# Optimization experiments

Measured on AMD Instinct MI355X. Metric: run time of the kernel, lower is better.

The kernel has to match this reference:

```python
import jax, jax.numpy as jnp
import numpy as np

B, N, DIM = 2, 16384, 512
H, D = 8, 64          # heads, dim_head
M = 64                # n_global_queries
SC, DC = 64, 64       # context slices, context_dim


def _linear(x, W, b):
    return x @ W.T + b


def setup_inputs() -> dict:
    key = jax.random.key(0)
    ks = jax.random.split(key, 12)
    def w(k, shape, fan_in):
        return jax.random.normal(k, shape, jnp.float32) / np.sqrt(fan_in)
    return {
        "x": jax.random.normal(ks[0], (B, N, DIM), jnp.float32),
        "context": jax.random.normal(ks[1], (B, H, SC, DC), jnp.float32),
        "q_global": jax.random.normal(ks[2], (1, H, M, D), jnp.float32),
        "Wx": w(ks[3], (H * D, DIM), DIM), "bx": jnp.zeros((H * D,), jnp.float32),
        "Wk": w(ks[4], (D, D), D), "bk": jnp.zeros((D,), jnp.float32),
        "Wv": w(ks[5], (D, D), D), "bv": jnp.zeros((D,), jnp.float32),
        "Wcq": w(ks[6], (D, D), D), "bcq": jnp.zeros((D,), jnp.float32),
        "Wck": w(ks[7], (D, DC), DC), "bck": jnp.zeros((D,), jnp.float32),
        "Wcv": w(ks[8], (D, DC), DC), "bcv": jnp.zeros((D,), jnp.float32),
        "state_mixing": jnp.zeros((), jnp.float32),
        "Wo": w(ks[9], (DIM, H * D), H * D), "bo": jnp.zeros((DIM,), jnp.float32),
    }


def reference(x, context, q_global, Wx, bx, Wk, bk, Wv, bv,
              Wcq, bcq, Wck, bck, Wcv, bcv, state_mixing, Wo, bo):
    scale = 1.0  # module uses self.scale = 1.0 (no 1/sqrt(d))
    b, n, _ = x.shape
    # in-projection: (B,N,C) -> (B,H,N,D)
    x_mid = _linear(x, Wx, bx).reshape(b, n, H, D).transpose(0, 2, 1, 3)

    # ---- FLARE low-rank self-attention (routing via M global queries) ----
    k = _linear(x_mid, Wk, bk)  # (B,H,N,D)
    v = _linear(x_mid, Wv, bv)  # (B,H,N,D)
    # encode: global queries attend over N tokens -> latent (B,H,M,D)
    enc = jax.nn.softmax(jnp.einsum('ghmd,bhnd->bhmn', q_global, k) * scale, axis=-1)
    latent = jnp.einsum('bhmn,bhnd->bhmd', enc, v)
    # decode: tokens (keys as queries) attend over M latents -> (B,H,N,D)
    dec = jax.nn.softmax(jnp.einsum('bhnd,ghmd->bhnm', k, q_global) * scale, axis=-1)
    self_attn = jnp.einsum('bhnm,bhmd->bhnd', dec, latent)

    # ---- cross-attention to geometry-aware context ----
    q = _linear(x_mid, Wcq, bcq)          # (B,H,N,D)
    kc = _linear(context, Wck, bck)       # (B,H,Sc,D)
    vc = _linear(context, Wcv, bcv)       # (B,H,Sc,D)
    attn = jax.nn.softmax(jnp.einsum('bhnd,bhsd->bhns', q, kc) * scale, axis=-1)
    cross_attn = jnp.einsum('bhns,bhsd->bhnd', attn, vc)

    # ---- sigmoid-gated mixing ----
    w = jax.nn.sigmoid(state_mixing)
    out = w * self_attn + (1.0 - w) * cross_attn  # (B,H,N,D)

    out = out.transpose(0, 2, 1, 3).reshape(b, n, H * D)
    return _linear(out, Wo, bo)  # (B,N,C); dropout=0 (eval)
```

## Files before the change

### kernel.cpp

```cpp
#include <hip/hip_runtime.h>


typedef unsigned short u16;
typedef __attribute__((ext_vector_type(4))) float  f32x4;
typedef __attribute__((ext_vector_type(4))) u16    u16x4;
typedef __attribute__((ext_vector_type(8))) __bf16 bf16x8;

__device__ __forceinline__ float bf2f(u16 u) {
    return __uint_as_float(((unsigned)u) << 16);
}
__device__ __forceinline__ u16 f2bf(float f) {
    unsigned u = __float_as_uint(f);
    u += 0x7fffu + ((u >> 16) & 1u);
    return (u16)(u >> 16);
}
__device__ __forceinline__ void gload16(const void* g, void* l) {
    __builtin_amdgcn_global_load_lds(
        (const __attribute__((address_space(1))) unsigned int*)g,
        (__attribute__((address_space(3))) unsigned int*)l, 16, 0, 0);
}

#define MASK_NONE 0x7fffffffu

template<int BM, int BN, int WMW, int WNW>
__device__ __forceinline__ void gemm_core(
    const u16* __restrict__ A, int lda, unsigned amask, int koffA,
    const u16* __restrict__ Bm, int ldb, unsigned bmask, int koffB,
    int K, int trow, int tcol,
    u16* As, u16* Bs,
    f32x4 (&acc)[BM / WMW / 16][BN / WNW / 16])
{
    constexpr int FM = BM / WMW / 16;
    constexpr int FN = BN / WNW / 16;
    const int tid  = threadIdx.x;
    const int wid  = tid >> 6, lane = tid & 63;
    const int wm   = wid % WMW, wn = wid / WMW;
    const int wr   = wm * (BM / WMW), wc = wn * (BN / WNW);
    const int lrow = lane & 15, lk = (lane >> 4) * 8;

    for (int kt = 0; kt < K; kt += 32) {
        __syncthreads();
#pragma unroll
        for (int i = 0; i < BM / 64; i++) {
            int c = i * 256 + tid;
            int row = c >> 2, kg = c & 3;
            unsigned kk = ((unsigned)(koffA + kt + kg * 8)) & amask;
            gload16(A + (size_t)(trow + row) * lda + kk, As + (size_t)c * 8);
        }
#pragma unroll
        for (int i = 0; i < BN / 64; i++) {
            int c = i * 256 + tid;
            int col = c >> 2, kg = c & 3;
            unsigned kk = ((unsigned)(koffB + kt + kg * 8)) & bmask;
            gload16(Bm + (size_t)(tcol + col) * ldb + kk, Bs + (size_t)c * 8);
        }
        __syncthreads();

        bf16x8 af[FM], bfr[FN];
#pragma unroll
        for (int fm = 0; fm < FM; fm++)
            af[fm] = *(const bf16x8*)&As[(wr + fm * 16 + lrow) * 32 + lk];
#pragma unroll
        for (int fn = 0; fn < FN; fn++)
            bfr[fn] = *(const bf16x8*)&Bs[(wc + fn * 16 + lrow) * 32 + lk];
#pragma unroll
        for (int fm = 0; fm < FM; fm++)
#pragma unroll
            for (int fn = 0; fn < FN; fn++)
                acc[fm][fn] = __builtin_amdgcn_mfma_f32_16x16x32_bf16(
                    af[fm], bfr[fn], acc[fm][fn], 0, 0, 0);
    }
}


__global__ void prep_x(const float* __restrict__ x, u16* __restrict__ xs)
{
    int t = blockIdx.x * 256 + threadIdx.x;
    int n = t >> 7, e4 = (t & 127) << 2;
    f32x4 v = *(const f32x4*)(x + (size_t)n * 512 + e4);
    u16x4 hi;
#pragma unroll
    for (int j = 0; j < 4; j++) hi[j] = f2bf(v[j]);
    *(u16x4*)(xs + (size_t)n * 512 + e4) = hi;
}

__global__ void prep_w(const float* Wk, const float* Wcq, const float* Wv,
                       const float* Wx, float* CKF, float* CQF, u16* wV)
{
    int idx = blockIdx.x * 256 + threadIdx.x;
    int which = idx >> 18;
    int rem = idx & 262143;
    int c = rem >> 9, e = rem & 511;
    int h = c >> 6, d = c & 63;
    const float* W = which == 0 ? Wk : (which == 1 ? Wcq : Wv);
    float s = 0.f;
#pragma unroll 8
    for (int j = 0; j < 64; j++)
        s += W[d * 64 + j] * Wx[(h * 64 + j) * 512 + e];
    if (which == 0)      CKF[(size_t)c * 512 + e] = s;
    else if (which == 1) CQF[(size_t)c * 512 + e] = s;
    else                 wV [(size_t)c * 512 + e] = f2bf(s);
}

__global__ void prep_bias(const float* Wk, const float* Wcq, const float* Wv,
                          const float* bk, const float* bcq, const float* bv,
                          const float* bx, float* biasKQ, float* biasV)
{
    int t = blockIdx.x * 256 + threadIdx.x;
    if (t < 1024) {
        const float* W  = (t < 512) ? Wk : Wcq;
        const float* bb = (t < 512) ? bk : bcq;
        int c = t & 511; int h = c >> 6, d = c & 63;
        float s = bb[d];
        for (int j = 0; j < 64; j++) s += W[d * 64 + j] * bx[h * 64 + j];
        biasKQ[t] = s;
    } else if (t < 1536) {
        int c = t - 1024; int h = c >> 6, d = c & 63;
        float s = bv[d];
        for (int j = 0; j < 64; j++) s += Wv[d * 64 + j] * bx[h * 64 + j];
        biasV[c] = s;
    }
}

__global__ void prep_ctx(const float* ctx, const float* Wck, const float* bck,
                         const float* Wcv, const float* bcv, const float* smix,
                         float* kcf, u16* vcT)
{
    int t = blockIdx.x * 256 + threadIdx.x;
    int bh = t >> 12, r = t & 4095;
    int s_ = r >> 6, d = r & 63;
    const float* crow = ctx + ((size_t)bh * 64 + s_) * 64;
    float kc = bck[d], vc = bcv[d];
#pragma unroll 8
    for (int e = 0; e < 64; e++) {
        float ce = crow[e];
        kc += ce * Wck[d * 64 + e];
        vc += ce * Wcv[d * 64 + e];
    }
    kcf[(size_t)bh * 4096 + s_ * 64 + d] = kc;
    float w = 1.f / (1.f + __expf(-smix[0]));
    int pos = (s_ & 15) * 4 + (s_ >> 4);
    vcT[(size_t)bh * 4096 + pos * 64 + d] = f2bf((1.f - w) * vc);
}

__global__ void prep_b2(const float* CKF, const float* CQF, const float* qg,
                        const float* kcf, const float* biasKQ, u16* BigB, float* CC)
{
    int idx = blockIdx.x * 256 + threadIdx.x;
    if (idx < 262144) {
        int hm = idx >> 9, e = idx & 511;
        int h = hm >> 6;
        float s = 0.f;
#pragma unroll 8
        for (int d = 0; d < 64; d++)
            s += CKF[(size_t)(h * 64 + d) * 512 + e] * qg[(size_t)hm * 64 + d];
        u16 hi = f2bf(s), lo = f2bf(s - bf2f(hi));
#pragma unroll
        for (int b = 0; b < 2; b++) {
            size_t base = (size_t)b * 1048576 + (size_t)hm * 1024;
            BigB[base + e]       = lo;
            BigB[base + 512 + e] = hi;
        }
    } else if (idx < 786432) {
        int i2 = idx - 262144;
        int r = i2 >> 9, e = i2 & 511;
        int b = r >> 9, hs = r & 511;
        int h = hs >> 6, s_ = hs & 63;
        float s = 0.f;
#pragma unroll 8
        for (int d = 0; d < 64; d++)
            s += CQF[(size_t)(h * 64 + d) * 512 + e]
               * kcf[(size_t)(b * 8 + h) * 4096 + s_ * 64 + d];
        u16 hi = f2bf(s), lo = f2bf(s - bf2f(hi));
        size_t base = (size_t)b * 1048576 + (size_t)(512 + hs) * 1024;
        BigB[base + e]       = lo;
        BigB[base + 512 + e] = hi;
    } else if (idx < 787968) {
        int t = idx - 786432;
        if (t < 512) {
            int h = t >> 6;
            float s = 0.f;
            for (int d = 0; d < 64; d++) s += biasKQ[h * 64 + d] * qg[(size_t)t * 64 + d];
            CC[t] = s; CC[1024 + t] = s;
        } else {
            int j = t - 512;
            int b = j >> 9, hs = j & 511;
            int h = hs >> 6, s_ = hs & 63;
            float s = 0.f;
            for (int d = 0; d < 64; d++)
                s += biasKQ[512 + h * 64 + d]
                   * kcf[(size_t)(b * 8 + h) * 4096 + s_ * 64 + d];
            CC[b * 1024 + 512 + hs] = s;
        }
    }
}

__global__ __launch_bounds__(256, 2) void k_vt(const u16* wV, const u16* xs,
                                               const float* biasV, u16* vT)
{
    __shared__ u16 As[128 * 32], Bs[128 * 32];
    f32x4 acc[4][4] = {};
    int b = blockIdx.z;
    int f = blockIdx.y * gridDim.x + blockIdx.x;
    int w = (f & 7) * 64 + (f >> 3);
    int trow = (w & 3) * 128;
    int tcol = (w >> 2) * 128;
    gemm_core<128, 128, 2, 2>(wV, 512, MASK_NONE, 0,
                              xs + (size_t)b * 8388608, 512, MASK_NONE, 0,
                              512, trow, tcol, As, Bs, acc);
    int tid = threadIdx.x, wid = tid >> 6, lane = tid & 63;
    int wr = (wid & 1) * 64, wc = (wid >> 1) * 64;
    int g = lane >> 4, li = lane & 15;
#pragma unroll
    for (int fm = 0; fm < 4; fm++)
#pragma unroll
        for (int fn = 0; fn < 4; fn++) {
            int col = tcol + wc + fn * 16 + li;
#pragma unroll
            for (int j = 0; j < 4; j++) {
                int a = trow + wr + fm * 16 + g * 4 + j;
                vT[((size_t)b * 512 + a) * 16384 + col] = f2bf(acc[fm][fn][j] + biasV[a]);
            }
        }
}

__global__ void k_L(const u16* xs, const u16* BigB, const float* CC,
                    u16* P12, float* DD)
{
    __shared__ u16 As[128 * 32], BsLo[128 * 32], BsHi[128 * 32];
    f32x4 acc[4][4] = {};
    int f = blockIdx.x;
    int w = (f & 7) * 256 + (f >> 3);
    int jt = w & 7, nb = w >> 3;
    int b = nb >> 7, ntile = nb & 127;
    int trow = ntile * 128, tcol = jt * 128;
    const u16* A  = xs   + (size_t)b * 8388608;
    const u16* Bm = BigB + (size_t)b * 1048576;
    int tid = threadIdx.x, wid = tid >> 6, lane = tid & 63;
    int wm = wid & 1, wn = wid >> 1;
    int wr = wm * 64, wc = wn * 64;
    int lrow = lane & 15, lk = (lane >> 4) * 8;

    for (int kt = 0; kt < 512; kt += 32) {
        __syncthreads();
#pragma unroll
        for (int i = 0; i < 2; i++) {
            int c = i * 256 + tid;
            int row = c >> 2, kg = c & 3;
            gload16(A + (size_t)(trow + row) * 512 + kt + kg * 8, As + (size_t)c * 8);
        }
#pragma unroll
        for (int i = 0; i < 2; i++) {
            int c = i * 256 + tid;
            int col = c >> 2, kg = c & 3;
            gload16(Bm + (size_t)(tcol + col) * 1024 + kt + kg * 8,
                    BsLo + (size_t)c * 8);
            gload16(Bm + (size_t)(tcol + col) * 1024 + 512 + kt + kg * 8,
                    BsHi + (size_t)c * 8);
        }
        __syncthreads();

        bf16x8 af[4], bfr[4];
#pragma unroll
        for (int fm = 0; fm < 4; fm++)
            af[fm] = *(const bf16x8*)&As[(wr + fm * 16 + lrow) * 32 + lk];
#pragma unroll
        for (int fn = 0; fn < 4; fn++)
            bfr[fn] = *(const bf16x8*)&BsLo[(wc + fn * 16 + lrow) * 32 + lk];
#pragma unroll
        for (int fm = 0; fm < 4; fm++)
#pragma unroll
            for (int fn = 0; fn < 4; fn++)
                acc[fm][fn] = __builtin_amdgcn_mfma_f32_16x16x32_bf16(
                    af[fm], bfr[fn], acc[fm][fn], 0, 0, 0);
#pragma unroll
        for (int fn = 0; fn < 4; fn++)
            bfr[fn] = *(const bf16x8*)&BsHi[(wc + fn * 16 + lrow) * 32 + lk];
#pragma unroll
        for (int fm = 0; fm < 4; fm++)
#pragma unroll
            for (int fn = 0; fn < 4; fn++)
                acc[fm][fn] = __builtin_amdgcn_mfma_f32_16x16x32_bf16(
                    af[fm], bfr[fn], acc[fm][fn], 0, 0, 0);
    }

    int g = lane >> 4, li = lane & 15;
    float cj[4];
#pragma unroll
    for (int fn = 0; fn < 4; fn++) cj[fn] = CC[b * 1024 + tcol + wc + fn * 16 + li];

    int h = jt * 2 + wn;
#pragma unroll
    for (int fm = 0; fm < 4; fm++)
#pragma unroll
        for (int j = 0; j < 4; j++) {
            float ev[4]; float dsum = 0.f;
#pragma unroll
            for (int fn = 0; fn < 4; fn++) {
                ev[fn] = __expf(acc[fm][fn][j] + cj[fn]);
                dsum += ev[fn];
            }
            dsum += __shfl_xor(dsum, 1); dsum += __shfl_xor(dsum, 2);
            dsum += __shfl_xor(dsum, 4); dsum += __shfl_xor(dsum, 8);
            float inv = 1.f / dsum;
            int row = trow + wr + fm * 16 + g * 4 + j;
            size_t pb = ((size_t)b * 16384 + row) * 1024 + tcol + wc;
            u16x4 pk;
#pragma unroll
            for (int fn = 0; fn < 4; fn++) pk[fn] = f2bf(ev[fn] * inv);
            *(u16x4*)(P12 + pb + li * 4) = pk;
            if (jt < 4 && li == 0)
                DD[(size_t)(b * 8 + h) * 16384 + row] = dsum;
        }
}

__global__ void k_dene(const u16* P12, const float* DD, float* denp)
{
    int blk = blockIdx.x;
    int b = blk >> 7, ch = blk & 127;
    int t = threadIdx.x;
    int h = t >> 5;
    float s0 = 0.f, s1 = 0.f;
    const float* ddb = DD + (size_t)(b * 8 + h) * 16384;
    const u16* base = P12 + (size_t)b * 16384 * 1024 + 2 * t;
    int n0 = ch * 128;
    for (int i = 0; i < 128; i++) {
        int n = n0 + i;
        unsigned v = *(const unsigned*)(base + (size_t)n * 1024);
        float dd = ddb[n];
        s0 += bf2f((u16)(v & 0xffff)) * dd;
        s1 += bf2f((u16)(v >> 16)) * dd;
    }
    denp[(size_t)(b * 512 + 2 * t) * 128 + ch]     = s0;
    denp[(size_t)(b * 512 + 2 * t + 1) * 128 + ch] = s1;
}

__global__ __launch_bounds__(256, 2) void k_latT(const u16* vT, const u16* P12,
                                                 const float* DD, float* latp)
{
    __shared__ u16 As[64 * 32], Bs[64 * 32];
    f32x4 acc[2][2] = {};
    int ch = blockIdx.x, bh = blockIdx.z;
    int b = bh >> 3, h = bh & 7;
    int koff = ch * 512;
    int tid = threadIdx.x, wid = tid >> 6, lane = tid & 63;
    int wr = (wid & 1) * 32, wc = (wid >> 1) * 32;
    int lrow = lane & 15, lk = (lane >> 4) * 8;
    const u16* Avt = vT + (size_t)bh * 64 * 16384;

    for (int kt = 0; kt < 512; kt += 32) {
        __syncthreads();
        {
            int row = tid >> 2, kg = tid & 3;
            gload16(Avt + (size_t)row * 16384 + koff + kt + kg * 8, As + (size_t)tid * 8);
        }
        {
            int nl = tid & 31, m0 = (tid >> 5) * 8;
            int n = koff + kt + nl;
            const u16* src = P12 + ((size_t)b * 16384 + n) * 1024 + h * 64 + m0;
            u16x4 p0 = *(const u16x4*)src;
            u16x4 p1 = *(const u16x4*)(src + 4);
            float ddv = DD[(size_t)bh * 16384 + n];
#pragma unroll
            for (int i = 0; i < 4; i++) {
                int m = m0 + i;
                Bs[m * 32 + (nl ^ ((m & 3) << 3))] = f2bf(bf2f(p0[i]) * ddv);
            }
#pragma unroll
            for (int i = 0; i < 4; i++) {
                int m = m0 + 4 + i;
                Bs[m * 32 + (nl ^ ((m & 3) << 3))] = f2bf(bf2f(p1[i]) * ddv);
            }
        }
        __syncthreads();
        bf16x8 af[2], bfv[2];
#pragma unroll
        for (int fm = 0; fm < 2; fm++)
            af[fm] = *(const bf16x8*)&As[(wr + fm * 16 + lrow) * 32 + lk];
#pragma unroll
        for (int fn = 0; fn < 2; fn++) {
            int m = wc + fn * 16 + lrow;
            bfv[fn] = *(const bf16x8*)&Bs[m * 32 + (lk ^ ((m & 3) << 3))];
        }
#pragma unroll
        for (int fm = 0; fm < 2; fm++)
#pragma unroll
            for (int fn = 0; fn < 2; fn++)
                acc[fm][fn] = __builtin_amdgcn_mfma_f32_16x16x32_bf16(
                    af[fm], bfv[fn], acc[fm][fn], 0, 0, 0);
    }
    float* C = latp + ((size_t)ch * 16 + bh) * 4096;
    int g = lane >> 4, li = lane & 15;
#pragma unroll
    for (int fm = 0; fm < 2; fm++)
#pragma unroll
        for (int fn = 0; fn < 2; fn++)
#pragma unroll
            for (int j = 0; j < 4; j++) {
                int row = wr + fm * 16 + g * 4 + j;
                int col = wc + fn * 16 + li;
                C[row * 64 + col] = acc[fm][fn][j];
            }
}

__global__ void k_latfin(const float* latp, const float* denp, const float* smix,
                         u16* latB)
{
    int t = blockIdx.x * 256 + threadIdx.x;
    int bh = t >> 12, r = t & 4095;
    int d = r >> 6, m = r & 63;
    int b = bh >> 3, h = bh & 7;
    float w = 1.f / (1.f + __expf(-smix[0]));
    float s = 0.f;
    for (int c = 0; c < 32; c++) s += latp[((size_t)c * 16 + bh) * 4096 + r];
    float dd = 0.f;
    const float* dp = denp + (size_t)(b * 512 + h * 64 + m) * 128;
    for (int c = 0; c < 128; c++) dd += dp[c];
    latB[(size_t)bh * 4096 + m * 64 + d] = f2bf(w * s / dd);
}

__global__ void prep_g(const u16* latB, const u16* vcT, const float* Wo, u16* G)
{
    int idx = blockIdx.x * 256 + threadIdx.x;
    int b = idx >> 19;
    int r = idx & 524287;
    int e = r >> 10, k = r & 1023;
    int h = (k >> 6) & 7, dm = k & 63;
    const u16* src = (k < 512) ? latB : vcT;
    const float* wrow = Wo + (size_t)e * 512 + h * 64;
    const u16* sb = src + (size_t)(b * 8 + h) * 4096 + dm * 64;
    float s = 0.f;
#pragma unroll
    for (int d0 = 0; d0 < 64; d0 += 4) {
        u16x4 sv = *(const u16x4*)(sb + d0);
        f32x4 wv = *(const f32x4*)(wrow + d0);
        s += bf2f(sv[0]) * wv[0] + bf2f(sv[1]) * wv[1]
           + bf2f(sv[2]) * wv[2] + bf2f(sv[3]) * wv[3];
    }
    G[(size_t)b * 524288 + (size_t)e * 1024 + k] = f2bf(s);
}

__global__ __launch_bounds__(256, 2) void k_fbig(const u16* P12, const u16* G,
                                                 const float* bo, float* out)
{
    __shared__ u16 As[128 * 32], Bs[128 * 32];
    f32x4 acc[4][4] = {};
    int f = blockIdx.y * gridDim.x + blockIdx.x;
    int w = (f & 7) * 128 + (f >> 3);
    int tcol = (w & 3) * 128, trow = (w >> 2) * 128;
    int b = trow >> 14;
    gemm_core<128, 128, 2, 2>(P12, 1024, MASK_NONE, 0,
                              G + (size_t)b * 524288, 1024, MASK_NONE, 0,
                              1024, trow, tcol, As, Bs, acc);
    int tid = threadIdx.x, wid = tid >> 6, lane = tid & 63;
    int wr = (wid & 1) * 64, wc = (wid >> 1) * 64;
    int g = lane >> 4, li = lane & 15;
#pragma unroll
    for (int fm = 0; fm < 4; fm++)
#pragma unroll
        for (int fn = 0; fn < 4; fn++) {
            int col = tcol + wc + fn * 16 + li;
            float bias = bo[col];
#pragma unroll
            for (int j = 0; j < 4; j++) {
                int row = trow + wr + fm * 16 + g * 4 + j;
                out[(size_t)row * 512 + col] = acc[fm][fn][j] + bias;
            }
        }
}

static const size_t XS_OFF   = 0;
static const size_t P12_OFF  = 33554432;
static const size_t VT_OFF   = 100663296;
static const size_t CKF_OFF  = 134217728;
static const size_t CQF_OFF  = 135266304;
static const size_t WV_OFF   = 136314880;
static const size_t BIGB_OFF = 136839168;
static const size_t KCF_OFF  = 141033472;
static const size_t VCT_OFF  = 141295616;
static const size_t BKQ_OFF  = 141426688;
static const size_t BV_OFF   = 141430784;
static const size_t CC_OFF   = 141432832;
static const size_t DENP_OFF = 141441024;
static const size_t DD_OFF   = 141965312;
static const size_t LATP_OFF = 143013888;
static const size_t LATB_OFF = 151402496;
static const size_t G_OFF    = 151533568;

extern "C" void kernel_launch(void* const* d_in, const int* in_sizes, int n_in,
                              void* d_out, int out_size, void* d_ws, size_t ws_size,
                              hipStream_t stream)
{
    const float* x    = (const float*)d_in[0];
    const float* ctx  = (const float*)d_in[1];
    const float* qg   = (const float*)d_in[2];
    const float* Wx   = (const float*)d_in[3];
    const float* bx   = (const float*)d_in[4];
    const float* Wk   = (const float*)d_in[5];
    const float* bk   = (const float*)d_in[6];
    const float* Wv   = (const float*)d_in[7];
    const float* bv   = (const float*)d_in[8];
    const float* Wcq  = (const float*)d_in[9];
    const float* bcq  = (const float*)d_in[10];
    const float* Wck  = (const float*)d_in[11];
    const float* bck  = (const float*)d_in[12];
    const float* Wcv  = (const float*)d_in[13];
    const float* bcv  = (const float*)d_in[14];
    const float* smix = (const float*)d_in[15];
    const float* Wo   = (const float*)d_in[16];
    const float* bo   = (const float*)d_in[17];

    char* ws = (char*)d_ws;
    u16*   xs    = (u16*)  (ws + XS_OFF);
    u16*   P12   = (u16*)  (ws + P12_OFF);
    u16*   vT    = (u16*)  (ws + VT_OFF);
    float* CKF   = (float*)(ws + CKF_OFF);
    float* CQF   = (float*)(ws + CQF_OFF);
    u16*   wV    = (u16*)  (ws + WV_OFF);
    u16*   BigB  = (u16*)  (ws + BIGB_OFF);
    float* kcf   = (float*)(ws + KCF_OFF);
    u16*   vcT   = (u16*)  (ws + VCT_OFF);
    float* biasKQ= (float*)(ws + BKQ_OFF);
    float* biasV = (float*)(ws + BV_OFF);
    float* CC    = (float*)(ws + CC_OFF);
    float* denp  = (float*)(ws + DENP_OFF);
    float* DD    = (float*)(ws + DD_OFF);
    float* latp  = (float*)(ws + LATP_OFF);
    u16*   latB  = (u16*)  (ws + LATB_OFF);
    u16*   G     = (u16*)  (ws + G_OFF);

    prep_w   <<< 3072, 256, 0, stream>>>(Wk, Wcq, Wv, Wx, CKF, CQF, wV);
    prep_bias<<<    6, 256, 0, stream>>>(Wk, Wcq, Wv, bk, bcq, bv, bx, biasKQ, biasV);
    prep_ctx <<<  256, 256, 0, stream>>>(ctx, Wck, bck, Wcv, bcv, smix, kcf, vcT);
    prep_x   <<<16384, 256, 0, stream>>>(x, xs);
    prep_b2  <<< 3078, 256, 0, stream>>>(CKF, CQF, qg, kcf, biasKQ, BigB, CC);

    k_vt    <<<dim3(128,   4, 2), 256, 0, stream>>>(wV, xs, biasV, vT);
    k_L     <<<2048, 256, 0, stream>>>(xs, BigB, CC, P12, DD);
    k_dene  <<< 256, 256, 0, stream>>>(P12, DD, denp);
    k_latT  <<<dim3( 32,   1, 16), 256, 0, stream>>>(vT, P12, DD, latp);
    k_latfin<<< 256, 256, 0, stream>>>(latp, denp, smix, latB);
    prep_g  <<<4096, 256, 0, stream>>>(latB, vcT, Wo, G);
    k_fbig  <<<dim3(  4, 256, 1), 256, 0, stream>>>(P12, G, bo, (float*)d_out);
}
```

Measured before the change: 269.7 us.

## Merge prep kernels, fold denominator sum into k_latT, use K=64 GEMM steps

Four prep kernels (x cast, weight folding, context projection, bias folding) are merged into one launch with block-range dispatch. The encode-softmax denominator reduction (k_dene), which re-read P12, is removed. Those row sums are now accumulated inside k_latT from values it already loads, so the denominator partials drop from 128 chunks to 32. The vt and final-output GEMMs now stage 64-wide K slices per barrier pair, doubling LDS per block, to halve the synchronisation count.

```diff
diff --git a/kernel.cpp b/kernel.cpp
--- a/kernel.cpp
+++ b/kernel.cpp
@@ -23,9 +23,9 @@
 #define MASK_NONE 0x7fffffffu
 
 template<int BM, int BN, int WMW, int WNW>
-__device__ __forceinline__ void gemm_core(
-    const u16* __restrict__ A, int lda, unsigned amask, int koffA,
-    const u16* __restrict__ Bm, int ldb, unsigned bmask, int koffB,
+__device__ __forceinline__ void gemm_core64(
+    const u16* __restrict__ A, int lda,
+    const u16* __restrict__ Bm, int ldb,
     int K, int trow, int tcol,
     u16* As, u16* Bs,
     f32x4 (&acc)[BM / WMW / 16][BN / WNW / 16])
@@ -38,109 +38,110 @@
     const int wr   = wm * (BM / WMW), wc = wn * (BN / WNW);
     const int lrow = lane & 15, lk = (lane >> 4) * 8;
 
-    for (int kt = 0; kt < K; kt += 32) {
+    for (int kt = 0; kt < K; kt += 64) {
         __syncthreads();
 #pragma unroll
-        for (int i = 0; i < BM / 64; i++) {
-            int c = i * 256 + tid;
-            int row = c >> 2, kg = c & 3;
-            unsigned kk = ((unsigned)(koffA + kt + kg * 8)) & amask;
-            gload16(A + (size_t)(trow + row) * lda + kk, As + (size_t)c * 8);
-        }
-#pragma unroll
-        for (int i = 0; i < BN / 64; i++) {
-            int c = i * 256 + tid;
-            int col = c >> 2, kg = c & 3;
-            unsigned kk = ((unsigned)(koffB + kt + kg * 8)) & bmask;
-            gload16(Bm + (size_t)(tcol + col) * ldb + kk, Bs + (size_t)c * 8);
+        for (int s = 0; s < 2; s++) {
+#pragma unroll
+            for (int i = 0; i < BM / 64; i++) {
+                int c = i * 256 + tid;
+                int row = c >> 2, kg = c & 3;
+                gload16(A + (size_t)(trow + row) * lda + kt + s * 32 + kg * 8,
+                        As + (size_t)s * BM * 32 + (size_t)c * 8);
+            }
+#pragma unroll
+            for (int i = 0; i < BN / 64; i++) {
+                int c = i * 256 + tid;
+                int col = c >> 2, kg = c & 3;
+                gload16(Bm + (size_t)(tcol + col) * ldb + kt + s * 32 + kg * 8,
+                        Bs + (size_t)s * BN * 32 + (size_t)c * 8);
+            }
         }
         __syncthreads();
 
-        bf16x8 af[FM], bfr[FN];
-#pragma unroll
-        for (int fm = 0; fm < FM; fm++)
-            af[fm] = *(const bf16x8*)&As[(wr + fm * 16 + lrow) * 32 + lk];
-#pragma unroll
-        for (int fn = 0; fn < FN; fn++)
-            bfr[fn] = *(const bf16x8*)&Bs[(wc + fn * 16 + lrow) * 32 + lk];
-#pragma unroll
-        for (int fm = 0; fm < FM; fm++)
+#pragma unroll
+        for (int s = 0; s < 2; s++) {
+            bf16x8 af[FM], bfr[FN];
+#pragma unroll
+            for (int fm = 0; fm < FM; fm++)
+                af[fm] = *(const bf16x8*)&As[s * BM * 32 + (wr + fm * 16 + lrow) * 32 + lk];
 #pragma unroll
             for (int fn = 0; fn < FN; fn++)
-                acc[fm][fn] = __builtin_amdgcn_mfma_f32_16x16x32_bf16(
-                    af[fm], bfr[fn], acc[fm][fn], 0, 0, 0);
-    }
-}
-
-
-__global__ void prep_x(const float* __restrict__ x, u16* __restrict__ xs)
-{
-    int t = blockIdx.x * 256 + threadIdx.x;
-    int n = t >> 7, e4 = (t & 127) << 2;
-    f32x4 v = *(const f32x4*)(x + (size_t)n * 512 + e4);
-    u16x4 hi;
-#pragma unroll
-    for (int j = 0; j < 4; j++) hi[j] = f2bf(v[j]);
-    *(u16x4*)(xs + (size_t)n * 512 + e4) = hi;
-}
-
-__global__ void prep_w(const float* Wk, const float* Wcq, const float* Wv,
-                       const float* Wx, float* CKF, float* CQF, u16* wV)
-{
-    int idx = blockIdx.x * 256 + threadIdx.x;
-    int which = idx >> 18;
-    int rem = idx & 262143;
-    int c = rem >> 9, e = rem & 511;
-    int h = c >> 6, d = c & 63;
-    const float* W = which == 0 ? Wk : (which == 1 ? Wcq : Wv);
-    float s = 0.f;
+                bfr[fn] = *(const bf16x8*)&Bs[s * BN * 32 + (wc + fn * 16 + lrow) * 32 + lk];
+#pragma unroll
+            for (int fm = 0; fm < FM; fm++)
+#pragma unroll
+                for (int fn = 0; fn < FN; fn++)
+                    acc[fm][fn] = __builtin_amdgcn_mfma_f32_16x16x32_bf16(
+                        af[fm], bfr[fn], acc[fm][fn], 0, 0, 0);
+        }
+    }
+}
+
+__global__ void prep_all(const float* x, const float* Wk, const float* Wcq,
+                         const float* Wv, const float* Wx,
+                         const float* bk, const float* bcq, const float* bv,
+                         const float* bx,
+                         const float* ctx, const float* Wck, const float* bck,
+                         const float* Wcv, const float* bcv, const float* smix,
+                         u16* xs, float* CKF, float* CQF, u16* wV,
+                         float* biasKQ, float* biasV, float* kcf, u16* vcT)
+{
+    int blk = blockIdx.x;
+    if (blk < 16384) {
+        int t = blk * 256 + threadIdx.x;
+        int n = t >> 7, e4 = (t & 127) << 2;
+        f32x4 v = *(const f32x4*)(x + (size_t)n * 512 + e4);
+        u16x4 hi;
+#pragma unroll
+        for (int j = 0; j < 4; j++) hi[j] = f2bf(v[j]);
+        *(u16x4*)(xs + (size_t)n * 512 + e4) = hi;
+    } else if (blk < 19456) {
+        int idx = (blk - 16384) * 256 + threadIdx.x;
+        int which = idx >> 18;
+        int rem = idx & 262143;
+        int c = rem >> 9, e = rem & 511;
+        int h = c >> 6, d = c & 63;
+        const float* W = which == 0 ? Wk : (which == 1 ? Wcq : Wv);
+        float s = 0.f;
 #pragma unroll 8
-    for (int j = 0; j < 64; j++)
-        s += W[d * 64 + j] * Wx[(h * 64 + j) * 512 + e];
-    if (which == 0)      CKF[(size_t)c * 512 + e] = s;
-    else if (which == 1) CQF[(size_t)c * 512 + e] = s;
-    else                 wV [(size_t)c * 512 + e] = f2bf(s);
-}
-
-__global__ void prep_bias(const float* Wk, const float* Wcq, const float* Wv,
-                          const float* bk, const float* bcq, const float* bv,
-                          const float* bx, float* biasKQ, float* biasV)
-{
-    int t = blockIdx.x * 256 + threadIdx.x;
-    if (t < 1024) {
-        const float* W  = (t < 512) ? Wk : Wcq;
-        const float* bb = (t < 512) ? bk : bcq;
-        int c = t & 511; int h = c >> 6, d = c & 63;
-        float s = bb[d];
-        for (int j = 0; j < 64; j++) s += W[d * 64 + j] * bx[h * 64 + j];
-        biasKQ[t] = s;
-    } else if (t < 1536) {
-        int c = t - 1024; int h = c >> 6, d = c & 63;
-        float s = bv[d];
-        for (int j = 0; j < 64; j++) s += Wv[d * 64 + j] * bx[h * 64 + j];
-        biasV[c] = s;
-    }
-}
-
-__global__ void prep_ctx(const float* ctx, const float* Wck, const float* bck,
-                         const float* Wcv, const float* bcv, const float* smix,
-                         float* kcf, u16* vcT)
-{
-    int t = blockIdx.x * 256 + threadIdx.x;
-    int bh = t >> 12, r = t & 4095;
-    int s_ = r >> 6, d = r & 63;
-    const float* crow = ctx + ((size_t)bh * 64 + s_) * 64;
-    float kc = bck[d], vc = bcv[d];
+        for (int j = 0; j < 64; j++)
+            s += W[d * 64 + j] * Wx[(h * 64 + j) * 512 + e];
+        if (which == 0)      CKF[(size_t)c * 512 + e] = s;
+        else if (which == 1) CQF[(size_t)c * 512 + e] = s;
+        else                 wV [(size_t)c * 512 + e] = f2bf(s);
+    } else if (blk < 19712) {
+        int t = (blk - 19456) * 256 + threadIdx.x;
+        int bh = t >> 12, r = t & 4095;
+        int s_ = r >> 6, d = r & 63;
+        const float* crow = ctx + ((size_t)bh * 64 + s_) * 64;
+        float kc = bck[d], vc = bcv[d];
 #pragma unroll 8
-    for (int e = 0; e < 64; e++) {
-        float ce = crow[e];
-        kc += ce * Wck[d * 64 + e];
-        vc += ce * Wcv[d * 64 + e];
-    }
-    kcf[(size_t)bh * 4096 + s_ * 64 + d] = kc;
-    float w = 1.f / (1.f + __expf(-smix[0]));
-    int pos = (s_ & 15) * 4 + (s_ >> 4);
-    vcT[(size_t)bh * 4096 + pos * 64 + d] = f2bf((1.f - w) * vc);
+        for (int e = 0; e < 64; e++) {
+            float ce = crow[e];
+            kc += ce * Wck[d * 64 + e];
+            vc += ce * Wcv[d * 64 + e];
+        }
+        kcf[(size_t)bh * 4096 + s_ * 64 + d] = kc;
+        float w = 1.f / (1.f + __expf(-smix[0]));
+        int pos = (s_ & 15) * 4 + (s_ >> 4);
+        vcT[(size_t)bh * 4096 + pos * 64 + d] = f2bf((1.f - w) * vc);
+    } else {
+        int t = (blk - 19712) * 256 + threadIdx.x;
+        if (t < 1024) {
+            const float* W  = (t < 512) ? Wk : Wcq;
+            const float* bb = (t < 512) ? bk : bcq;
+            int c = t & 511; int h = c >> 6, d = c & 63;
+            float s = bb[d];
+            for (int j = 0; j < 64; j++) s += W[d * 64 + j] * bx[h * 64 + j];
+            biasKQ[t] = s;
+        } else if (t < 1536) {
+            int c = t - 1024; int h = c >> 6, d = c & 63;
+            float s = bv[d];
+            for (int j = 0; j < 64; j++) s += Wv[d * 64 + j] * bx[h * 64 + j];
+            biasV[c] = s;
+        }
+    }
 }
 
 __global__ void prep_b2(const float* CKF, const float* CQF, const float* qg,
@@ -198,16 +199,15 @@
 __global__ __launch_bounds__(256, 2) void k_vt(const u16* wV, const u16* xs,
                                                const float* biasV, u16* vT)
 {
-    __shared__ u16 As[128 * 32], Bs[128 * 32];
+    __shared__ u16 As[128 * 64], Bs[128 * 64];
     f32x4 acc[4][4] = {};
     int b = blockIdx.z;
     int f = blockIdx.y * gridDim.x + blockIdx.x;
     int w = (f & 7) * 64 + (f >> 3);
     int trow = (w & 3) * 128;
     int tcol = (w >> 2) * 128;
-    gemm_core<128, 128, 2, 2>(wV, 512, MASK_NONE, 0,
-                              xs + (size_t)b * 8388608, 512, MASK_NONE, 0,
-                              512, trow, tcol, As, Bs, acc);
+    gemm_core64<128, 128, 2, 2>(wV, 512, xs + (size_t)b * 8388608, 512,
+                                512, trow, tcol, As, Bs, acc);
     int tid = threadIdx.x, wid = tid >> 6, lane = tid & 63;
     int wr = (wid & 1) * 64, wc = (wid >> 1) * 64;
     int g = lane >> 4, li = lane & 15;
@@ -314,32 +314,15 @@
         }
 }
 
-__global__ void k_dene(const u16* P12, const float* DD, float* denp)
-{
-    int blk = blockIdx.x;
-    int b = blk >> 7, ch = blk & 127;
-    int t = threadIdx.x;
-    int h = t >> 5;
-    float s0 = 0.f, s1 = 0.f;
-    const float* ddb = DD + (size_t)(b * 8 + h) * 16384;
-    const u16* base = P12 + (size_t)b * 16384 * 1024 + 2 * t;
-    int n0 = ch * 128;
-    for (int i = 0; i < 128; i++) {
-        int n = n0 + i;
-        unsigned v = *(const unsigned*)(base + (size_t)n * 1024);
-        float dd = ddb[n];
-        s0 += bf2f((u16)(v & 0xffff)) * dd;
-        s1 += bf2f((u16)(v >> 16)) * dd;
-    }
-    denp[(size_t)(b * 512 + 2 * t) * 128 + ch]     = s0;
-    denp[(size_t)(b * 512 + 2 * t + 1) * 128 + ch] = s1;
-}
-
 __global__ __launch_bounds__(256, 2) void k_latT(const u16* vT, const u16* P12,
-                                                 const float* DD, float* latp)
-{
-    __shared__ u16 As[64 * 32], Bs[64 * 32];
+                                                 const float* DD, float* latp,
+                                                 float* denp)
+{
+    __shared__ u16 sh2[4096];
+    u16* As = sh2;
+    u16* Bs = sh2 + 2048;
     f32x4 acc[2][2] = {};
+    float dacc[8] = {0.f, 0.f, 0.f, 0.f, 0.f, 0.f, 0.f, 0.f};
     int ch = blockIdx.x, bh = blockIdx.z;
     int b = bh >> 3, h = bh & 7;
     int koff = ch * 512;
@@ -347,6 +330,7 @@
     int wr = (wid & 1) * 32, wc = (wid >> 1) * 32;
     int lrow = lane & 15, lk = (lane >> 4) * 8;
     const u16* Avt = vT + (size_t)bh * 64 * 16384;
+    int nl = tid & 31, m0 = (tid >> 5) * 8;
 
     for (int kt = 0; kt < 512; kt += 32) {
         __syncthreads();
@@ -355,7 +339,6 @@
             gload16(Avt + (size_t)row * 16384 + koff + kt + kg * 8, As + (size_t)tid * 8);
         }
         {
-            int nl = tid & 31, m0 = (tid >> 5) * 8;
             int n = koff + kt + nl;
             const u16* src = P12 + ((size_t)b * 16384 + n) * 1024 + h * 64 + m0;
             u16x4 p0 = *(const u16x4*)src;
@@ -364,12 +347,16 @@
 #pragma unroll
             for (int i = 0; i < 4; i++) {
                 int m = m0 + i;
-                Bs[m * 32 + (nl ^ ((m & 3) << 3))] = f2bf(bf2f(p0[i]) * ddv);
+                float v = bf2f(p0[i]) * ddv;
+                dacc[i] += v;
+                Bs[m * 32 + (nl ^ ((m & 3) << 3))] = f2bf(v);
             }
 #pragma unroll
             for (int i = 0; i < 4; i++) {
                 int m = m0 + 4 + i;
-                Bs[m * 32 + (nl ^ ((m & 3) << 3))] = f2bf(bf2f(p1[i]) * ddv);
+                float v = bf2f(p1[i]) * ddv;
+                dacc[4 + i] += v;
+                Bs[m * 32 + (nl ^ ((m & 3) << 3))] = f2bf(v);
             }
         }
         __syncthreads();
@@ -401,6 +388,18 @@
                 int col = wc + fn * 16 + li;
                 C[row * 64 + col] = acc[fm][fn][j];
             }
+    __syncthreads();
+    float* red = (float*)sh2;
+#pragma unroll
+    for (int i = 0; i < 8; i++)
+        red[(m0 + i) * 32 + nl] = dacc[i];
+    __syncthreads();
+    if (tid < 64) {
+        float s = 0.f;
+        const float* rr = red + tid * 32;
+        for (int j = 0; j < 32; j++) s += rr[j];
+        denp[(size_t)(bh * 64 + tid) * 32 + ch] = s;
+    }
 }
 
 __global__ void k_latfin(const float* latp, const float* denp, const float* smix,
@@ -409,13 +408,12 @@
     int t = blockIdx.x * 256 + threadIdx.x;
     int bh = t >> 12, r = t & 4095;
     int d = r >> 6, m = r & 63;
-    int b = bh >> 3, h = bh & 7;
     float w = 1.f / (1.f + __expf(-smix[0]));
     float s = 0.f;
     for (int c = 0; c < 32; c++) s += latp[((size_t)c * 16 + bh) * 4096 + r];
     float dd = 0.f;
-    const float* dp = denp + (size_t)(b * 512 + h * 64 + m) * 128;
-    for (int c = 0; c < 128; c++) dd += dp[c];
+    const float* dp = denp + (size_t)(bh * 64 + m) * 32;
+    for (int c = 0; c < 32; c++) dd += dp[c];
     latB[(size_t)bh * 4096 + m * 64 + d] = f2bf(w * s / dd);
 }
 
@@ -443,15 +441,14 @@
 __global__ __launch_bounds__(256, 2) void k_fbig(const u16* P12, const u16* G,
                                                  const float* bo, float* out)
 {
-    __shared__ u16 As[128 * 32], Bs[128 * 32];
+    __shared__ u16 As[128 * 64], Bs[128 * 64];
     f32x4 acc[4][4] = {};
     int f = blockIdx.y * gridDim.x + blockIdx.x;
     int w = (f & 7) * 128 + (f >> 3);
     int tcol = (w & 3) * 128, trow = (w >> 2) * 128;
     int b = trow >> 14;
-    gemm_core<128, 128, 2, 2>(P12, 1024, MASK_NONE, 0,
-                              G + (size_t)b * 524288, 1024, MASK_NONE, 0,
-                              1024, trow, tcol, As, Bs, acc);
+    gemm_core64<128, 128, 2, 2>(P12, 1024, G + (size_t)b * 524288, 1024,
+                                1024, trow, tcol, As, Bs, acc);
     int tid = threadIdx.x, wid = tid >> 6, lane = tid & 63;
     int wr = (wid & 1) * 64, wc = (wid >> 1) * 64;
     int g = lane >> 4, li = lane & 15;
@@ -529,16 +526,14 @@
     u16*   latB  = (u16*)  (ws + LATB_OFF);
     u16*   G     = (u16*)  (ws + G_OFF);
 
-    prep_w   <<< 3072, 256, 0, stream>>>(Wk, Wcq, Wv, Wx, CKF, CQF, wV);
-    prep_bias<<<    6, 256, 0, stream>>>(Wk, Wcq, Wv, bk, bcq, bv, bx, biasKQ, biasV);
-    prep_ctx <<<  256, 256, 0, stream>>>(ctx, Wck, bck, Wcv, bcv, smix, kcf, vcT);
-    prep_x   <<<16384, 256, 0, stream>>>(x, xs);
-    prep_b2  <<< 3078, 256, 0, stream>>>(CKF, CQF, qg, kcf, biasKQ, BigB, CC);
+    prep_all<<<19718, 256, 0, stream>>>(x, Wk, Wcq, Wv, Wx, bk, bcq, bv, bx,
+                                        ctx, Wck, bck, Wcv, bcv, smix,
+                                        xs, CKF, CQF, wV, biasKQ, biasV, kcf, vcT);
+    prep_b2 <<< 3078, 256, 0, stream>>>(CKF, CQF, qg, kcf, biasKQ, BigB, CC);
 
     k_vt    <<<dim3(128,   4, 2), 256, 0, stream>>>(wV, xs, biasV, vT);
     k_L     <<<2048, 256, 0, stream>>>(xs, BigB, CC, P12, DD);
-    k_dene  <<< 256, 256, 0, stream>>>(P12, DD, denp);
-    k_latT  <<<dim3( 32,   1, 16), 256, 0, stream>>>(vT, P12, DD, latp);
+    k_latT  <<<dim3( 32,   1, 16), 256, 0, stream>>>(vT, P12, DD, latp, denp);
     k_latfin<<< 256, 256, 0, stream>>>(latp, denp, smix, latB);
     prep_g  <<<4096, 256, 0, stream>>>(latB, vcT, Wo, G);
     k_fbig  <<<dim3(  4, 256, 1), 256, 0, stream>>>(P12, G, bo, (float*)d_out);
```

Result: faster. 250.2 us (-7.2%).
